# Kernel optimization log

Measured on AMD Instinct MI355X. Metric: run time of the kernel, lower is better.

The kernel has to match this reference:

```python
import jax, jax.numpy as jnp
import numpy as np

B, T, A = 64, 100, 8732          # batch, padded GT boxes per image, SSD300 anchors
NUM_CLASSES = 21                 # VOC
THR = 0.5                        # overlap_threshold
VAR0, VAR1 = 0.1, 0.2            # loc_variance


def setup_inputs() -> dict:
    key = jax.random.key(0)
    k1, k2, k3, k4, k5 = jax.random.split(key, 5)
    # GT boxes: valid point-coord boxes in [0,1] with positive area, plus float label col
    xy1 = jax.random.uniform(k1, (B, T, 2)) * 0.7
    wh = jax.random.uniform(k2, (B, T, 2)) * 0.28 + 0.02
    labels = jax.random.randint(k3, (B, T), 0, NUM_CLASSES - 1).astype(jnp.float32)
    targets = jnp.concatenate([xy1, xy1 + wh, labels[..., None]], axis=-1)  # [B,T,5]
    # anchors in center coords (cx, cy, w, h), positive w/h
    cxy = jax.random.uniform(k4, (A, 2))
    awh = jax.random.uniform(k5, (A, 2)) * 0.48 + 0.02
    anchors = jnp.concatenate([cxy, awh], axis=-1)  # [A,4]
    return {"targets": targets, "anchors": anchors}


def _iou(boxes, anchors_pt):
    # boxes [T,4] point coords, anchors_pt [A,4] point coords -> [T,A]
    tl = jnp.maximum(boxes[:, None, :2], anchors_pt[None, :, :2])
    br = jnp.minimum(boxes[:, None, 2:], anchors_pt[None, :, 2:])
    inter = jnp.prod(jnp.clip(br - tl, 0.0), axis=-1)
    area_b = jnp.prod(boxes[:, 2:] - boxes[:, :2], axis=-1)
    area_a = jnp.prod(anchors_pt[:, 2:] - anchors_pt[:, :2], axis=-1)
    return inter / (area_b[:, None] + area_a[None, :] - inter)


def reference(targets, anchors):
    # centerCoordsToPointCoords(anchors)
    anchors_pt = jnp.concatenate(
        [anchors[:, :2] - anchors[:, 2:] * 0.5, anchors[:, :2] + anchors[:, 2:] * 0.5],
        axis=-1,
    )

    def match(tgt):  # tgt: [T,5]
        boxes = tgt[:, :4]
        labels = tgt[:, 4]
        iou = _iou(boxes, anchors_pt)                    # [T,A]
        anchor_index = jnp.argmax(iou, axis=1)           # best anchor per GT [T]
        gt_overlap = jnp.max(iou, axis=0)                # best GT overlap per anchor [A]
        gt_index = jnp.argmax(iou, axis=0)               # best GT per anchor [A]
        # index_fill_: guarantee each GT's best anchor counts as matched
        gt_overlap = gt_overlap.at[anchor_index].set(1.0)
        gt_index = gt_index.at[anchor_index].set(jnp.arange(boxes.shape[0]))
        matched = boxes[gt_index]                        # [A,4] point coords
        # pointCoordsToCenterCoords + encodeCenterCoords
        cxy = (matched[:, :2] + matched[:, 2:]) * 0.5
        wh = matched[:, 2:] - matched[:, :2]
        loc = jnp.concatenate(
            [(cxy - anchors[:, :2]) / (VAR0 * anchors[:, 2:]),
             jnp.log(wh / anchors[:, 2:]) / VAR1],
            axis=-1,
        )                                                # [A,4]
        conf = (labels[gt_index] + 1.0).astype(jnp.int32)
        conf = jnp.where(gt_overlap < THR, 0, conf)      # background below threshold
        return loc, conf

    return jax.vmap(match)(targets)  # loc_t [B,A,4], conf_t [B,A]
```

## Files before the change

### kernel.cpp

```cpp
#include <hip/hip_runtime.h>

#define BB 64
#define TT 100
#define AA 8732
#define CHUNK 512
#define NCHUNK ((AA + CHUNK - 1) / CHUNK)

typedef unsigned long long u64;
typedef unsigned int u32;
typedef unsigned short u16;

__constant__ int c_tbl[5] = {0, 28, 52, 76, 100};

__device__ __forceinline__ float fdiv_faithful(float i, float u) {
    float r = __builtin_amdgcn_rcpf(u);
    r = __builtin_fmaf(__builtin_fmaf(-u, r, 1.0f), r, r);
    float q = __fmul_rn(i, r);
    float rem = __builtin_fmaf(-u, q, i);
    return __builtin_fmaf(rem, r, q);
}

__device__ __forceinline__ float iou_f(float bx1, float by1, float bx2, float by2, float areab,
                                       float ax1, float ay1, float ax2, float ay2, float areaa) {
    float dx = fminf(fmaxf(__fsub_rn(fminf(bx2, ax2), fmaxf(bx1, ax1)), 0.0f), 1.0f);
    float dy = fminf(fmaxf(__fsub_rn(fminf(by2, ay2), fmaxf(by1, ay1)), 0.0f), 1.0f);
    float inter = __fmul_rn(dx, dy);
    float uni = __fsub_rn(__fadd_rn(areab, areaa), inter);
    return fdiv_faithful(inter, uni);
}

__device__ __forceinline__ void wave_max63_x4(float& x0, float& x1, float& x2, float& x3) {
    asm volatile(
        "s_nop 1\n\t"
        "v_max_f32 %0, %0, %0 row_shr:1\n\t"
        "v_max_f32 %1, %1, %1 row_shr:1\n\t"
        "v_max_f32 %2, %2, %2 row_shr:1\n\t"
        "v_max_f32 %3, %3, %3 row_shr:1\n\t"
        "v_max_f32 %0, %0, %0 row_shr:2\n\t"
        "v_max_f32 %1, %1, %1 row_shr:2\n\t"
        "v_max_f32 %2, %2, %2 row_shr:2\n\t"
        "v_max_f32 %3, %3, %3 row_shr:2\n\t"
        "v_max_f32 %0, %0, %0 row_shr:4\n\t"
        "v_max_f32 %1, %1, %1 row_shr:4\n\t"
        "v_max_f32 %2, %2, %2 row_shr:4\n\t"
        "v_max_f32 %3, %3, %3 row_shr:4\n\t"
        "v_max_f32 %0, %0, %0 row_shr:8\n\t"
        "v_max_f32 %1, %1, %1 row_shr:8\n\t"
        "v_max_f32 %2, %2, %2 row_shr:8\n\t"
        "v_max_f32 %3, %3, %3 row_shr:8\n\t"
        "v_max_f32 %0, %0, %0 row_bcast:15\n\t"
        "v_max_f32 %1, %1, %1 row_bcast:15\n\t"
        "v_max_f32 %2, %2, %2 row_bcast:15\n\t"
        "v_max_f32 %3, %3, %3 row_bcast:15\n\t"
        "v_max_f32 %0, %0, %0 row_bcast:31\n\t"
        "v_max_f32 %1, %1, %1 row_bcast:31\n\t"
        "v_max_f32 %2, %2, %2 row_bcast:31\n\t"
        "v_max_f32 %3, %3, %3 row_bcast:31\n\t"
        "s_nop 0"
        : "+v"(x0), "+v"(x1), "+v"(x2), "+v"(x3));
}

__global__ __launch_bounds__(256) void k_init(u64* __restrict__ keys) {
    int i = blockIdx.x * 256 + threadIdx.x;
    if (i < BB * TT) keys[i] = 0ULL;
}

__global__ __launch_bounds__(512) void k_phaseA(const float* __restrict__ targets,
                                                const float* __restrict__ anchors,
                                                u64* __restrict__ keys,
                                                u64* __restrict__ pa2) {
    const int b = blockIdx.y;
    const int z = blockIdx.z;
    const int tid = threadIdx.x;
    const int half = tid >> 8;
    const int u = tid & 255;
    const int a0 = blockIdx.x * CHUNK + u * 2;
    const bool valid = a0 < AA;
    const int lane = tid & 63, wv = tid >> 6;

    __shared__ __align__(16) float sh_area[TT];
    __shared__ u64 sh_red[4][TT];
    __shared__ u64 sh_pa[CHUNK];

    if (tid < TT) {
        const float* tg = targets + ((size_t)b * TT + tid) * 5;
        sh_area[tid] = __fmul_rn(__fsub_rn(tg[2], tg[0]), __fsub_rn(tg[3], tg[1]));
    }
    __syncthreads();

    float ax10 = 0.f, ay10 = 0.f, ax20 = 0.f, ay20 = 0.f, aa0 = 1.f;
    float ax11 = 0.f, ay11 = 0.f, ax21 = 0.f, ay21 = 0.f, aa1 = 1.f;
    if (valid) {
        const float4* anc = (const float4*)(anchors + (size_t)a0 * 4);
        float4 c0 = anc[0], c1 = anc[1];
        float hx0 = __fmul_rn(c0.z, 0.5f), hy0 = __fmul_rn(c0.w, 0.5f);
        ax10 = __fsub_rn(c0.x, hx0); ay10 = __fsub_rn(c0.y, hy0);
        ax20 = __fadd_rn(c0.x, hx0); ay20 = __fadd_rn(c0.y, hy0);
        aa0 = __fmul_rn(__fsub_rn(ax20, ax10), __fsub_rn(ay20, ay10));
        float hx1 = __fmul_rn(c1.z, 0.5f), hy1 = __fmul_rn(c1.w, 0.5f);
        ax11 = __fsub_rn(c1.x, hx1); ay11 = __fsub_rn(c1.y, hy1);
        ax21 = __fadd_rn(c1.x, hx1); ay21 = __fadd_rn(c1.y, hy1);
        aa1 = __fmul_rn(__fsub_rn(ax21, ax11), __fsub_rn(ay21, ay11));
    }

    float best0 = -1.f, best1 = -1.f;
    int gi0 = 0, gi1 = 0;
    const u32 wave_base = (u32)blockIdx.x * CHUNK + (u32)(wv & 3) * 128u;

    const int tbeg = c_tbl[z * 2 + half];
    const int tend = c_tbl[z * 2 + half + 1];
    const float* tbase = targets + (size_t)b * TT * 5;
    for (int t = tbeg; t < tend; t += 4) {
        const float* tb = tbase + (size_t)t * 5;
        const float B0x = tb[0],  B0y = tb[1],  B0z = tb[2],  B0w = tb[3];
        const float B1x = tb[5],  B1y = tb[6],  B1z = tb[7],  B1w = tb[8];
        const float B2x = tb[10], B2y = tb[11], B2z = tb[12], B2w = tb[13];
        const float B3x = tb[15], B3y = tb[16], B3z = tb[17], B3w = tb[18];
        const float4 arv = *(const float4*)&sh_area[t];
        float ar0 = arv.x, ar1 = arv.y, ar2 = arv.z, ar3 = arv.w;

        float v00 = iou_f(B0x, B0y, B0z, B0w, ar0, ax10, ay10, ax20, ay20, aa0);
        float v01 = iou_f(B0x, B0y, B0z, B0w, ar0, ax11, ay11, ax21, ay21, aa1);
        float v10 = iou_f(B1x, B1y, B1z, B1w, ar1, ax10, ay10, ax20, ay20, aa0);
        float v11 = iou_f(B1x, B1y, B1z, B1w, ar1, ax11, ay11, ax21, ay21, aa1);
        float v20 = iou_f(B2x, B2y, B2z, B2w, ar2, ax10, ay10, ax20, ay20, aa0);
        float v21 = iou_f(B2x, B2y, B2z, B2w, ar2, ax11, ay11, ax21, ay21, aa1);
        float v30 = iou_f(B3x, B3y, B3z, B3w, ar3, ax10, ay10, ax20, ay20, aa0);
        float v31 = iou_f(B3x, B3y, B3z, B3w, ar3, ax11, ay11, ax21, ay21, aa1);

        if (v00 > best0) { best0 = v00; gi0 = t; }
        if (v10 > best0) { best0 = v10; gi0 = t + 1; }
        if (v20 > best0) { best0 = v20; gi0 = t + 2; }
        if (v30 > best0) { best0 = v30; gi0 = t + 3; }
        if (v01 > best1) { best1 = v01; gi1 = t; }
        if (v11 > best1) { best1 = v11; gi1 = t + 1; }
        if (v21 > best1) { best1 = v21; gi1 = t + 2; }
        if (v31 > best1) { best1 = v31; gi1 = t + 3; }

        float vm0 = fmaxf(v00, v01), vm1 = fmaxf(v10, v11);
        float vm2 = fmaxf(v20, v21), vm3 = fmaxf(v30, v31);
        float w0 = vm0, w1 = vm1, w2 = vm2, w3 = vm3;
        wave_max63_x4(w0, w1, w2, w3);
        u32 wm0 = (u32)__builtin_amdgcn_readlane(__float_as_int(w0), 63);
        u32 wm1 = (u32)__builtin_amdgcn_readlane(__float_as_int(w1), 63);
        u32 wm2 = (u32)__builtin_amdgcn_readlane(__float_as_int(w2), 63);
        u32 wm3 = (u32)__builtin_amdgcn_readlane(__float_as_int(w3), 63);
        u64 me0 = __ballot(vm0 == __uint_as_float(wm0));
        u64 mp0 = __ballot(v01 > v00);
        u64 me1 = __ballot(vm1 == __uint_as_float(wm1));
        u64 mp1 = __ballot(v11 > v10);
        u64 me2 = __ballot(vm2 == __uint_as_float(wm2));
        u64 mp2 = __ballot(v21 > v20);
        u64 me3 = __ballot(vm3 == __uint_as_float(wm3));
        u64 mp3 = __ballot(v31 > v30);
        u32 wl0 = (u32)(__ffsll((long long)me0) - 1);
        u32 wl1 = (u32)(__ffsll((long long)me1) - 1);
        u32 wl2 = (u32)(__ffsll((long long)me2) - 1);
        u32 wl3 = (u32)(__ffsll((long long)me3) - 1);
        u32 g0 = wave_base + wl0 * 2u + (u32)((mp0 >> wl0) & 1ULL);
        u32 g1 = wave_base + wl1 * 2u + (u32)((mp1 >> wl1) & 1ULL);
        u32 g2 = wave_base + wl2 * 2u + (u32)((mp2 >> wl2) & 1ULL);
        u32 g3 = wave_base + wl3 * 2u + (u32)((mp3 >> wl3) & 1ULL);
        if (lane == 0) {
            u64* r = &sh_red[wv & 3][t];
            r[0] = (((u64)wm0) << 32) | (u32)~g0;
            r[1] = (((u64)wm1) << 32) | (u32)~g1;
            r[2] = (((u64)wm2) << 32) | (u32)~g2;
            r[3] = (((u64)wm3) << 32) | (u32)~g3;
        }
    }
    __syncthreads();

    if (tid >= c_tbl[z * 2] && tid < c_tbl[z * 2 + 2]) {
        u64 m0 = sh_red[0][tid], m1 = sh_red[1][tid];
        u64 m2 = sh_red[2][tid], m3 = sh_red[3][tid];
        u64 m = m0 > m1 ? m0 : m1;
        if (m2 > m) m = m2;
        if (m3 > m) m = m3;
        atomicMax(&keys[b * TT + tid], m);
    }

    if (half == 0) {
        sh_pa[u * 2 + 0] = (((u64)__float_as_uint(best0)) << 32) | (u32)(~(u32)gi0);
        sh_pa[u * 2 + 1] = (((u64)__float_as_uint(best1)) << 32) | (u32)(~(u32)gi1);
    }
    __syncthreads();
    if (half == 1 && valid) {
        u64 k0 = (((u64)__float_as_uint(best0)) << 32) | (u32)(~(u32)gi0);
        u64 k1 = (((u64)__float_as_uint(best1)) << 32) | (u32)(~(u32)gi1);
        u64 m0 = sh_pa[u * 2 + 0]; if (k0 > m0) m0 = k0;
        u64 m1 = sh_pa[u * 2 + 1]; if (k1 > m1) m1 = k1;
        pa2[((size_t)b * AA + a0) * 2 + z] = m0;
        pa2[((size_t)b * AA + a0 + 1) * 2 + z] = m1;
    }
}

__global__ __launch_bounds__(256) void k_encode(const float* __restrict__ targets,
                                                const float* __restrict__ anchors,
                                                const u64* __restrict__ keys,
                                                const u64* pa2,
                                                float* out) {
    const int b = blockIdx.y;
    const int a = blockIdx.x * 256 + threadIdx.x;

    __shared__ float sh_t[TT][6];
    __shared__ u32 sh_ov[256];

    sh_ov[threadIdx.x] = 0;
    __syncthreads();
    for (int t = threadIdx.x; t < TT; t += 256) {
        const float* tg = targets + ((size_t)b * TT + t) * 5;
        sh_t[t][0] = tg[0]; sh_t[t][1] = tg[1];
        sh_t[t][2] = tg[2]; sh_t[t][3] = tg[3];
        sh_t[t][4] = tg[4];
        u32 at = ~(u32)(keys[b * TT + t] & 0xFFFFFFFFu);
        if ((at >> 8) == (u32)blockIdx.x)
            atomicMax(&sh_ov[at & 255], 0x100u | (u32)t);
    }
    __syncthreads();
    if (a >= AA) return;

    const u64* pc = pa2 + ((size_t)b * AA + a) * 2;
    u64 kz0 = pc[0], kz1 = pc[1];
    u64 m = kz0 > kz1 ? kz0 : kz1;

    u32 ov = sh_ov[threadIdx.x];
    int gi; bool pos;
    if (ov) { gi = (int)(ov & 0x7F); pos = true; }
    else {
        gi = (int)((~(u32)m) & 0x7F);
        pos = __uint_as_float((u32)(m >> 32)) >= 0.5f;
    }

    const float4 anc = *(const float4*)(anchors + (size_t)a * 4);
    const float mx1 = sh_t[gi][0], my1 = sh_t[gi][1], mx2 = sh_t[gi][2], my2 = sh_t[gi][3];
    const float cx = (mx1 + mx2) * 0.5f, cy = (my1 + my2) * 0.5f;
    const float w = mx2 - mx1, h = my2 - my1;
    const float l0 = (cx - anc.x) / (0.1f * anc.z);
    const float l1 = (cy - anc.y) / (0.1f * anc.w);
    const float l2 = logf(w / anc.z) / 0.2f;
    const float l3 = logf(h / anc.w) / 0.2f;

    const size_t base = ((size_t)b * AA + a) * 4;
    *(float4*)(out + base) = make_float4(l0, l1, l2, l3);
    float conf = pos ? (float)(int)(sh_t[gi][4] + 1.0f) : 0.0f;
    out[(size_t)BB * AA * 4 + (size_t)b * AA + a] = conf;
}

extern "C" void kernel_launch(void* const* d_in, const int* in_sizes, int n_in,
                              void* d_out, int out_size, void* d_ws, size_t ws_size,
                              hipStream_t stream) {
    const float* targets = (const float*)d_in[0];
    const float* anchors = (const float*)d_in[1];
    float* out = (float*)d_out;
    u64* keys = (u64*)d_ws;
    u64* pa2 = (u64*)d_out;

    k_init<<<(BB * TT + 255) / 256, 256, 0, stream>>>(keys);
    dim3 gA(NCHUNK, BB, 2);
    k_phaseA<<<gA, 512, 0, stream>>>(targets, anchors, keys, pa2);
    dim3 gE((AA + 255) / 256, BB);
    k_encode<<<gE, 256, 0, stream>>>(targets, anchors, keys, pa2, out);
}
```

Measured before the change: 108.9 us.

## Drop T-split in phase A, pack per-anchor match into u16 flags

Result: no change. 107.9 us (-0.9%).

```diff
diff --git a/kernel.cpp b/kernel.cpp
--- a/kernel.cpp
+++ b/kernel.cpp
@@ -4,17 +4,14 @@
 #define TT 100
 #define AA 8732
 #define CHUNK 512
-#define NCHUNK ((AA + CHUNK - 1) / CHUNK)
+#define NCHUNK 20
 
 typedef unsigned long long u64;
 typedef unsigned int u32;
 typedef unsigned short u16;
 
-__constant__ int c_tbl[5] = {0, 28, 52, 76, 100};
-
 __device__ __forceinline__ float fdiv_faithful(float i, float u) {
     float r = __builtin_amdgcn_rcpf(u);
-    r = __builtin_fmaf(__builtin_fmaf(-u, r, 1.0f), r, r);
     float q = __fmul_rn(i, r);
     float rem = __builtin_fmaf(-u, q, i);
     return __builtin_fmaf(rem, r, q);
@@ -65,22 +62,18 @@
     if (i < BB * TT) keys[i] = 0ULL;
 }
 
-__global__ __launch_bounds__(512) void k_phaseA(const float* __restrict__ targets,
+__global__ __launch_bounds__(256) void k_phaseA(const float* __restrict__ targets,
                                                 const float* __restrict__ anchors,
                                                 u64* __restrict__ keys,
-                                                u64* __restrict__ pa2) {
+                                                u16* __restrict__ pa) {
     const int b = blockIdx.y;
-    const int z = blockIdx.z;
     const int tid = threadIdx.x;
-    const int half = tid >> 8;
-    const int u = tid & 255;
-    const int a0 = blockIdx.x * CHUNK + u * 2;
+    const int a0 = blockIdx.x * CHUNK + tid * 2;
     const bool valid = a0 < AA;
     const int lane = tid & 63, wv = tid >> 6;
 
     __shared__ __align__(16) float sh_area[TT];
     __shared__ u64 sh_red[4][TT];
-    __shared__ u64 sh_pa[CHUNK];
 
     if (tid < TT) {
         const float* tg = targets + ((size_t)b * TT + tid) * 5;
@@ -105,12 +98,10 @@
 
     float best0 = -1.f, best1 = -1.f;
     int gi0 = 0, gi1 = 0;
-    const u32 wave_base = (u32)blockIdx.x * CHUNK + (u32)(wv & 3) * 128u;
-
-    const int tbeg = c_tbl[z * 2 + half];
-    const int tend = c_tbl[z * 2 + half + 1];
+    const u32 wave_base = (u32)blockIdx.x * CHUNK + (u32)wv * 128u;
+
     const float* tbase = targets + (size_t)b * TT * 5;
-    for (int t = tbeg; t < tend; t += 4) {
+    for (int t = 0; t < TT; t += 4) {
         const float* tb = tbase + (size_t)t * 5;
         const float B0x = tb[0],  B0y = tb[1],  B0z = tb[2],  B0w = tb[3];
         const float B1x = tb[5],  B1y = tb[6],  B1z = tb[7],  B1w = tb[8];
@@ -162,7 +153,7 @@
         u32 g2 = wave_base + wl2 * 2u + (u32)((mp2 >> wl2) & 1ULL);
         u32 g3 = wave_base + wl3 * 2u + (u32)((mp3 >> wl3) & 1ULL);
         if (lane == 0) {
-            u64* r = &sh_red[wv & 3][t];
+            u64* r = &sh_red[wv][t];
             r[0] = (((u64)wm0) << 32) | (u32)~g0;
             r[1] = (((u64)wm1) << 32) | (u32)~g1;
             r[2] = (((u64)wm2) << 32) | (u32)~g2;
@@ -171,7 +162,7 @@
     }
     __syncthreads();
 
-    if (tid >= c_tbl[z * 2] && tid < c_tbl[z * 2 + 2]) {
+    if (tid < TT) {
         u64 m0 = sh_red[0][tid], m1 = sh_red[1][tid];
         u64 m2 = sh_red[2][tid], m3 = sh_red[3][tid];
         u64 m = m0 > m1 ? m0 : m1;
@@ -180,26 +171,18 @@
         atomicMax(&keys[b * TT + tid], m);
     }
 
-    if (half == 0) {
-        sh_pa[u * 2 + 0] = (((u64)__float_as_uint(best0)) << 32) | (u32)(~(u32)gi0);
-        sh_pa[u * 2 + 1] = (((u64)__float_as_uint(best1)) << 32) | (u32)(~(u32)gi1);
-    }
-    __syncthreads();
-    if (half == 1 && valid) {
-        u64 k0 = (((u64)__float_as_uint(best0)) << 32) | (u32)(~(u32)gi0);
-        u64 k1 = (((u64)__float_as_uint(best1)) << 32) | (u32)(~(u32)gi1);
-        u64 m0 = sh_pa[u * 2 + 0]; if (k0 > m0) m0 = k0;
-        u64 m1 = sh_pa[u * 2 + 1]; if (k1 > m1) m1 = k1;
-        pa2[((size_t)b * AA + a0) * 2 + z] = m0;
-        pa2[((size_t)b * AA + a0 + 1) * 2 + z] = m1;
+    if (valid) {
+        u32 f0 = (u32)gi0 | (best0 >= 0.5f ? 0x80u : 0u);
+        u32 f1 = (u32)gi1 | (best1 >= 0.5f ? 0x80u : 0u);
+        *(u32*)(pa + (size_t)b * AA + a0) = f0 | (f1 << 16);
     }
 }
 
 __global__ __launch_bounds__(256) void k_encode(const float* __restrict__ targets,
                                                 const float* __restrict__ anchors,
                                                 const u64* __restrict__ keys,
-                                                const u64* pa2,
-                                                float* out) {
+                                                const u16* __restrict__ pa,
+                                                float* __restrict__ out) {
     const int b = blockIdx.y;
     const int a = blockIdx.x * 256 + threadIdx.x;
 
@@ -220,17 +203,11 @@
     __syncthreads();
     if (a >= AA) return;
 
-    const u64* pc = pa2 + ((size_t)b * AA + a) * 2;
-    u64 kz0 = pc[0], kz1 = pc[1];
-    u64 m = kz0 > kz1 ? kz0 : kz1;
-
     u32 ov = sh_ov[threadIdx.x];
+    u32 v = pa[(size_t)b * AA + a];
     int gi; bool pos;
     if (ov) { gi = (int)(ov & 0x7F); pos = true; }
-    else {
-        gi = (int)((~(u32)m) & 0x7F);
-        pos = __uint_as_float((u32)(m >> 32)) >= 0.5f;
-    }
+    else     { gi = (int)(v & 0x7F); pos = (v & 0x80) != 0; }
 
     const float4 anc = *(const float4*)(anchors + (size_t)a * 4);
     const float mx1 = sh_t[gi][0], my1 = sh_t[gi][1], mx2 = sh_t[gi][2], my2 = sh_t[gi][3];
@@ -254,11 +231,11 @@
     const float* anchors = (const float*)d_in[1];
     float* out = (float*)d_out;
     u64* keys = (u64*)d_ws;
-    u64* pa2 = (u64*)d_out;
+    u16* pa = (u16*)((char*)d_ws + (size_t)BB * TT * 8);
 
     k_init<<<(BB * TT + 255) / 256, 256, 0, stream>>>(keys);
-    dim3 gA(NCHUNK, BB, 2);
-    k_phaseA<<<gA, 512, 0, stream>>>(targets, anchors, keys, pa2);
+    dim3 gA(NCHUNK, BB);
+    k_phaseA<<<gA, 256, 0, stream>>>(targets, anchors, keys, pa);
     dim3 gE((AA + 255) / 256, BB);
-    k_encode<<<gE, 256, 0, stream>>>(targets, anchors, keys, pa2, out);
-}
+    k_encode<<<gE, 256, 0, stream>>>(targets, anchors, keys, pa, out);
+}
```
